# Kernel tuning notes

Measured on AMD Instinct MI355X. Metric: run time of the kernel, lower is better.

## Reference

```python
import jax, jax.numpy as jnp
import numpy as np

N, E = 50000, 800000
H, C_HID = 4, 64  # heads, hidden_units
C_IN, C_OUT = 256, 64
NEG_SLOPE = 0.2
EPS = 1e-16


def gat_conv(x, src, dst, W, att_src, att_dst, bias):
    """PyG GATConv with concat=False (mean over heads) + bias.
    x: [N, F_in], W: [F_in, H*C], att_*: [H, C], bias: [C]."""
    n = x.shape[0]
    h = (x @ W).reshape(n, H, -1)                     # [N, H, C]
    a_src = jnp.sum(h * att_src, axis=-1)             # [N, H]
    a_dst = jnp.sum(h * att_dst, axis=-1)             # [N, H]
    e = jax.nn.leaky_relu(a_src[src] + a_dst[dst], NEG_SLOPE)  # [E, H]
    # segment softmax grouped by destination node
    m = jax.ops.segment_max(e, dst, num_segments=n)   # [N, H]
    e = jnp.exp(e - m[dst])
    denom = jax.ops.segment_sum(e, dst, num_segments=n)
    alpha = e / (denom[dst] + EPS)                    # [E, H]
    msg = h[src] * alpha[:, :, None]                  # [E, H, C]
    out = jax.ops.segment_sum(msg, dst, num_segments=n)  # [N, H, C]
    return out.mean(axis=1) + bias                    # concat=False -> head mean


def setup_inputs() -> dict:
    key = jax.random.key(0)
    ks = jax.random.split(key, 16)
    inp = {
        "x": jax.random.normal(ks[0], (N, C_IN), dtype=jnp.float32),
        "edge_index": jax.random.randint(ks[1], (2, E), 0, N, dtype=jnp.int64),
    }
    dims = [(C_IN, C_HID), (C_HID, C_HID), (C_HID, C_OUT)]
    for i, (fi, fo) in enumerate(dims, start=1):
        inp[f"W{i}"] = jax.random.normal(ks[2 + 4 * (i - 1)], (fi, H * fo), dtype=jnp.float32) * (1.0 / np.sqrt(fi))
        inp[f"as{i}"] = jax.random.normal(ks[3 + 4 * (i - 1)], (H, fo), dtype=jnp.float32) * 0.1
        inp[f"ad{i}"] = jax.random.normal(ks[4 + 4 * (i - 1)], (H, fo), dtype=jnp.float32) * 0.1
        inp[f"b{i}"] = jnp.zeros((fo,), dtype=jnp.float32)
    return inp


def reference(x, edge_index, W1, as1, ad1, b1, W2, as2, ad2, b2, W3, as3, ad3, b3):
    n = x.shape[0]
    loop = jnp.arange(n, dtype=edge_index.dtype)
    src = jnp.concatenate([edge_index[0], loop])  # add_self_loops=True (PyG default)
    dst = jnp.concatenate([edge_index[1], loop])
    layers = [(W1, as1, ad1, b1), (W2, as2, ad2, b2), (W3, as3, ad3, b3)]
    for (W, a_s, a_d, b) in layers:
        x = gat_conv(x, src, dst, W, a_s, a_d, b)
        x = jax.nn.relu(x)  # dropout is identity at inference
    return jax.nn.log_softmax(x, axis=-1)
```

## Files before the change

### kernel.cpp

```cpp
#include <hip/hip_runtime.h>
#include <hip/hip_bf16.h>
#include <math.h>
#include <stdint.h>

#define HEADS 4
#define CH 64
#define HC 256
#define NEG 0.2f
#define EPSV 1e-16f
#define NEGBIG -3.0e38f

typedef __attribute__((ext_vector_type(8))) short short8;
typedef __attribute__((ext_vector_type(4))) float f32x4;
typedef _Float16 f16_t;
typedef __fp16 fp16x2 __attribute__((ext_vector_type(2)));

__device__ __forceinline__ float lrelu(float x) { return x > 0.f ? x : NEG * x; }

__device__ __forceinline__ unsigned short f2bf(float f) {
  __hip_bfloat16 b = __float2bfloat16(f);
  return *reinterpret_cast<unsigned short*>(&b);
}
__device__ __forceinline__ unsigned short f16b(float f) {
  return __builtin_bit_cast(unsigned short, (f16_t)f);
}
__device__ __forceinline__ float dot2acc(unsigned int a, unsigned int h, float acc) {
#if __has_builtin(__builtin_amdgcn_fdot2)
  return __builtin_amdgcn_fdot2(__builtin_bit_cast(fp16x2, a),
                                __builtin_bit_cast(fp16x2, h), acc, false);
#else
  fp16x2 av = __builtin_bit_cast(fp16x2, a);
  fp16x2 hv = __builtin_bit_cast(fp16x2, h);
  return acc + (float)av[0] * (float)hv[0] + (float)av[1] * (float)hv[1];
#endif
}

__global__ __launch_bounds__(256) void wprep3_k(const float* __restrict__ W0,
                                                const float* __restrict__ W1,
                                                const float* __restrict__ W2,
                                                unsigned short* __restrict__ T0,
                                                unsigned short* __restrict__ T1,
                                                unsigned short* __restrict__ T2) {
  int i = blockIdx.x * 256 + threadIdx.x;
  if (i < 65536) {
    int k = i >> 8, n = i & 255;
    T0[n * 256 + k] = f2bf(W0[i]);
  } else if (i < 81920) {
    int j = i - 65536, k = j >> 8, n = j & 255;
    T1[n * 64 + k] = f2bf(W1[j]);
  } else if (i < 98304) {
    int j = i - 81920, k = j >> 8, n = j & 255;
    T2[n * 64 + k] = f2bf(W2[j]);
  }
}

#define AS_STR 268
#define CS_STR 258
template <int K, int AF32>
__global__ __launch_bounds__(256, 4) void mfma_gat_k(const float* __restrict__ Af,
                                                     const unsigned short* __restrict__ Ab,
                                                     const unsigned short* __restrict__ Wt,
                                                     const float* __restrict__ att_s,
                                                     const float* __restrict__ att_d,
                                                     unsigned short* __restrict__ ht16,
                                                     float* __restrict__ a_src,
                                                     float* __restrict__ a_dst,
                                                     int M) {
  __shared__ unsigned short Sh[32 * AS_STR];

  int tid = threadIdx.x;
  int bm = blockIdx.x * 32;
  int w = tid >> 6, l = tid & 63;
  int lr = l & 15, lk = l >> 4;
  int row_s = tid >> 3, seg = tid & 7;
  bool rowok = (bm + row_s < M);

  if (AF32) {
    #pragma unroll 4
    for (int kq = 0; kq < K; kq += 32) {
      float4 v = make_float4(0.f, 0.f, 0.f, 0.f);
      if (rowok)
        v = *reinterpret_cast<const float4*>(Af + (size_t)(bm + row_s) * K + kq + seg * 4);
      ushort4 u;
      u.x = f2bf(v.x); u.y = f2bf(v.y); u.z = f2bf(v.z); u.w = f2bf(v.w);
      *reinterpret_cast<ushort4*>(&Sh[row_s * AS_STR + kq + seg * 4]) = u;
    }
  } else {
    #pragma unroll 4
    for (int kq = 0; kq < K; kq += 32) {
      ushort4 u = make_ushort4(0, 0, 0, 0);
      if (rowok)
        u = *reinterpret_cast<const ushort4*>(Ab + (size_t)(bm + row_s) * K + kq + seg * 4);
      *reinterpret_cast<ushort4*>(&Sh[row_s * AS_STR + kq + seg * 4]) = u;
    }
  }
  __syncthreads();

  f32x4 acc[2][4];
  #pragma unroll
  for (int rt = 0; rt < 2; ++rt)
    #pragma unroll
    for (int ct = 0; ct < 4; ++ct) {
      f32x4 z = {0.f, 0.f, 0.f, 0.f};
      acc[rt][ct] = z;
    }

  const unsigned short* wp0 = Wt + (size_t)(w * 64 + lr) * K + lk * 8;

  #pragma unroll 2
  for (int k0 = 0; k0 < K; k0 += 32) {
    short8 bfr[4];
    #pragma unroll
    for (int ct = 0; ct < 4; ++ct)
      bfr[ct] = *reinterpret_cast<const short8*>(wp0 + (size_t)ct * 16 * K + k0);
    #pragma unroll
    for (int rt = 0; rt < 2; ++rt) {
      short8 af = *reinterpret_cast<const short8*>(&Sh[(rt * 16 + lr) * AS_STR + k0 + lk * 8]);
      #pragma unroll
      for (int ct = 0; ct < 4; ++ct)
        acc[rt][ct] = __builtin_amdgcn_mfma_f32_16x16x32_bf16(af, bfr[ct], acc[rt][ct], 0, 0, 0);
    }
  }
  __syncthreads();

  #pragma unroll
  for (int rt = 0; rt < 2; ++rt)
    #pragma unroll
    for (int ct = 0; ct < 4; ++ct)
      #pragma unroll
      for (int r = 0; r < 4; ++r) {
        int row = rt * 16 + lk * 4 + r;
        int c = ct * 16 + lr;
        Sh[row * CS_STR + c * 4 + w] = f16b(acc[rt][ct][r]);
      }
  __syncthreads();

  if (rowok) {
    ushort4* dst = reinterpret_cast<ushort4*>(ht16 + (size_t)(bm + row_s) * HC + seg * 32);
    const unsigned short* srcp = &Sh[row_s * CS_STR + seg * 32];
    #pragma unroll
    for (int q = 0; q < 4; ++q)
      dst[q] = *reinterpret_cast<const ushort4*>(srcp + q * 4);
  }

  {
    int nd = tid >> 3, q = tid & 7, h = q >> 1, half = q & 1;
    float ps = 0.f, pd = 0.f;
    const float* ats = att_s + h * 64 + half * 32;
    const float* atd = att_d + h * 64 + half * 32;
    const unsigned short* cp = &Sh[nd * CS_STR + (half * 32) * 4 + h];
    #pragma unroll
    for (int c = 0; c < 32; ++c) {
      float hv = (float)__builtin_bit_cast(f16_t, cp[c * 4]);
      ps += hv * ats[c];
      pd += hv * atd[c];
    }
    ps += __shfl_xor(ps, 1);
    pd += __shfl_xor(pd, 1);
    if (!(q & 1) && bm + nd < M) {
      a_src[(size_t)(bm + nd) * 4 + h] = ps;
      a_dst[(size_t)(bm + nd) * 4 + h] = pd;
    }
  }
}

__global__ __launch_bounds__(256) void hist_k(const int* __restrict__ dst, int* __restrict__ count, int E) {
  int e = blockIdx.x * blockDim.x + threadIdx.x;
  if (e < E) atomicAdd(&count[dst[e]], 1);
}

__global__ __launch_bounds__(512) void scan1_k(const int* __restrict__ count,
                                               int* __restrict__ rp,
                                               int* __restrict__ bsum, int n) {
  __shared__ int sh[512];
  int tx = threadIdx.x;
  int i = blockIdx.x * 512 + tx;
  int v = (i < n) ? count[i] : 0;
  sh[tx] = v;
  __syncthreads();
  #pragma unroll
  for (int off = 1; off < 512; off <<= 1) {
    int t = (tx >= off) ? sh[tx - off] : 0;
    __syncthreads();
    sh[tx] += t;
    __syncthreads();
  }
  if (i < n) rp[i] = sh[tx] - v;
  if (tx == 511) bsum[blockIdx.x] = sh[511];
}

__global__ __launch_bounds__(128) void scan2_k(int* __restrict__ bsum, int nb) {
  __shared__ int sh[128];
  int tx = threadIdx.x;
  int v = (tx < nb) ? bsum[tx] : 0;
  sh[tx] = v;
  __syncthreads();
  #pragma unroll
  for (int off = 1; off < 128; off <<= 1) {
    int t = (tx >= off) ? sh[tx - off] : 0;
    __syncthreads();
    sh[tx] += t;
    __syncthreads();
  }
  if (tx < nb) bsum[tx] = sh[tx] - v;
}

__global__ __launch_bounds__(512) void scan3_k(int* __restrict__ rp, const int* __restrict__ bsum,
                                               int n, int E) {
  int i = blockIdx.x * 512 + threadIdx.x;
  if (i < n) rp[i] += bsum[blockIdx.x];
  if (i == 0) rp[n] = E;
}

__global__ __launch_bounds__(256) void scatter_k(const int* __restrict__ src, const int* __restrict__ dst,
                                                 const int* __restrict__ rp, int* __restrict__ cursor,
                                                 int* __restrict__ csr_src, int E) {
  int e = blockIdx.x * blockDim.x + threadIdx.x;
  if (e >= E) return;
  int d = dst[e];
  int pos = rp[d] + atomicAdd(&cursor[d], 1);
  csr_src[pos] = src[e];
}

__global__ __launch_bounds__(256) void soft_agg_k(const int* __restrict__ rp,
                                                  const int* __restrict__ csr_src,
                                                  const float* __restrict__ a_src,
                                                  const float* __restrict__ a_dst,
                                                  const unsigned short* __restrict__ ht16,
                                                  const float* __restrict__ bias,
                                                  float* __restrict__ outf,
                                                  unsigned short* __restrict__ outb,
                                                  int N, int do_lsm) {
  __shared__ uint4 rec[4][34];
  int tid  = threadIdx.x;
  int w    = tid >> 6;
  int lane = tid & 63;
  int wid  = (blockIdx.x * blockDim.x + tid) >> 6;
  if (wid >= N) return;
  int rs = rp[wid], re = rp[wid + 1];
  int ep = lane & 15;
  int h  = lane >> 4;

  float adh = a_dst[(size_t)wid * 4 + h];
  float ash = a_src[(size_t)wid * 4 + h];
  float es  = lrelu(ash + adh);

  int s0 = 0, s1 = 0;
  float e0 = NEGBIG, e1 = NEGBIG;
  if (rs + ep < re) {
    s0 = csr_src[rs + ep];
    e0 = lrelu(a_src[(size_t)s0 * 4 + h] + adh);
  }
  if (rs + 16 + ep < re) {
    s1 = csr_src[rs + 16 + ep];
    e1 = lrelu(a_src[(size_t)s1 * 4 + h] + adh);
  }
  float m = fmaxf(es, fmaxf(e0, e1));
  for (int base = rs + 32; base < re; base += 16) {
    if (base + ep < re) {
      int s = csr_src[base + ep];
      m = fmaxf(m, lrelu(a_src[(size_t)s * 4 + h] + adh));
    }
  }
  #pragma unroll
  for (int off = 8; off > 0; off >>= 1) m = fmaxf(m, __shfl_xor(m, off));

  float p0 = expf(e0 - m), p1 = expf(e1 - m);
  float dn = p0 + p1;
  for (int base = rs + 32; base < re; base += 16) {
    if (base + ep < re) {
      int s = csr_src[base + ep];
      dn += expf(lrelu(a_src[(size_t)s * 4 + h] + adh) - m);
    }
  }
  #pragma unroll
  for (int off = 8; off > 0; off >>= 1) dn += __shfl_xor(dn, off);
  float sp = expf(es - m);
  dn += sp;
  float rr = 1.f / (dn + EPSV);

  unsigned short* recb = reinterpret_cast<unsigned short*>(&rec[w][0]);
  float acc = 0.f;
  const unsigned short* hl = ht16 + lane * 4;

  auto agg = [&](int cnt) {
    int k = 0;
    for (; k + 4 <= cnt; k += 4) {
      uint4 r0 = rec[w][k + 0], r1 = rec[w][k + 1];
      uint4 r2 = rec[w][k + 2], r3 = rec[w][k + 3];
      int t0 = __builtin_amdgcn_readfirstlane((int)r0.z);
      int t1 = __builtin_amdgcn_readfirstlane((int)r1.z);
      int t2 = __builtin_amdgcn_readfirstlane((int)r2.z);
      int t3 = __builtin_amdgcn_readfirstlane((int)r3.z);
      uint2 h0 = *reinterpret_cast<const uint2*>(hl + (size_t)t0 * HC);
      uint2 h1 = *reinterpret_cast<const uint2*>(hl + (size_t)t1 * HC);
      uint2 h2 = *reinterpret_cast<const uint2*>(hl + (size_t)t2 * HC);
      uint2 h3 = *reinterpret_cast<const uint2*>(hl + (size_t)t3 * HC);
      acc = dot2acc(r0.x, h0.x, acc); acc = dot2acc(r0.y, h0.y, acc);
      acc = dot2acc(r1.x, h1.x, acc); acc = dot2acc(r1.y, h1.y, acc);
      acc = dot2acc(r2.x, h2.x, acc); acc = dot2acc(r2.y, h2.y, acc);
      acc = dot2acc(r3.x, h3.x, acc); acc = dot2acc(r3.y, h3.y, acc);
    }
    for (; k < cnt; ++k) {
      uint4 r0 = rec[w][k];
      int t0 = __builtin_amdgcn_readfirstlane((int)r0.z);
      uint2 hv = *reinterpret_cast<const uint2*>(hl + (size_t)t0 * HC);
      acc = dot2acc(r0.x, hv.x, acc);
      acc = dot2acc(r0.y, hv.y, acc);
    }
  };

  if (ep == 0) recb[32 * 8 + h] = f16b(sp * rr);
  recb[ep * 8 + h] = f16b(p0 * rr);
  recb[(16 + ep) * 8 + h] = f16b(p1 * rr);
  if (h == 0) {
    *reinterpret_cast<int*>(recb + ep * 8 + 4) = s0;
    *reinterpret_cast<int*>(recb + (16 + ep) * 8 + 4) = s1;
  }
  {
    int cnt = re - rs; if (cnt > 32) cnt = 32;
    agg(cnt);
  }
  for (int base = rs + 32; base < re; base += 16) {
    int s = 0;
    float e = NEGBIG;
    if (base + ep < re) {
      s = csr_src[base + ep];
      e = lrelu(a_src[(size_t)s * 4 + h] + adh);
    }
    recb[ep * 8 + h] = f16b(expf(e - m) * rr);
    if (h == 0) *reinterpret_cast<int*>(recb + ep * 8 + 4) = s;
    int cnt = re - base; if (cnt > 16) cnt = 16;
    agg(cnt);
  }

  uint2 sa = *reinterpret_cast<const uint2*>(&rec[w][32]);
  uint2 shv = *reinterpret_cast<const uint2*>(ht16 + (size_t)wid * HC + lane * 4);
  acc = dot2acc(sa.x, shv.x, acc);
  acc = dot2acc(sa.y, shv.y, acc);
  float v = acc * 0.25f + bias[lane];
  v = fmaxf(v, 0.f);
  if (do_lsm) {
    float mx = v;
    #pragma unroll
    for (int off = 32; off > 0; off >>= 1) mx = fmaxf(mx, __shfl_xor(mx, off));
    float ex = expf(v - mx);
    float sm = ex;
    #pragma unroll
    for (int off = 32; off > 0; off >>= 1) sm += __shfl_xor(sm, off);
    outf[(size_t)wid * CH + lane] = v - mx - logf(sm);
  } else {
    outb[(size_t)wid * CH + lane] = f2bf(v);
  }
}

extern "C" void kernel_launch(void* const* d_in, const int* in_sizes, int n_in,
                              void* d_out, int out_size, void* d_ws, size_t ws_size,
                              hipStream_t stream) {
  const float* x0 = (const float*)d_in[0];
  const int*   ei = (const int*)d_in[1];
  int N = in_sizes[0] / HC;
  int E = in_sizes[1] / 2;
  const int* srcp = ei;
  const int* dstp = ei + E;

  const float* W[3]  = {(const float*)d_in[2], (const float*)d_in[6],  (const float*)d_in[10]};
  const float* AS[3] = {(const float*)d_in[3], (const float*)d_in[7],  (const float*)d_in[11]};
  const float* AD[3] = {(const float*)d_in[4], (const float*)d_in[8],  (const float*)d_in[12]};
  const float* BI[3] = {(const float*)d_in[5], (const float*)d_in[9],  (const float*)d_in[13]};

  char* ws = (char*)d_ws;
  size_t off = 0;
  auto alloc = [&](size_t bytes) {
    void* p = ws + off;
    off += (bytes + 255) & ~(size_t)255;
    return p;
  };
  unsigned short* ht16    = (unsigned short*)alloc((size_t)N * HC * 2);
  unsigned short* xb16    = (unsigned short*)alloc((size_t)N * CH * 2);
  float*          a_s     = (float*)alloc((size_t)N * 4 * 4);
  float*          a_d     = (float*)alloc((size_t)N * 4 * 4);
  int*            rowp    = (int*)alloc((size_t)(N + 1) * 4);
  int*            cursor  = (int*)alloc((size_t)N * 4);
  int*            csr_src = (int*)alloc((size_t)E * 4);
  int*            bsum    = (int*)alloc(512 * 4);
  unsigned short* Wt[3];
  Wt[0] = (unsigned short*)alloc((size_t)256 * 256 * 2);
  Wt[1] = (unsigned short*)alloc((size_t)256 * 64 * 2);
  Wt[2] = (unsigned short*)alloc((size_t)256 * 64 * 2);

  wprep3_k<<<384, 256, 0, stream>>>(W[0], W[1], W[2], Wt[0], Wt[1], Wt[2]);

  int nb = (N + 511) / 512;
  hipMemsetAsync(rowp, 0, (size_t)((char*)(cursor + N) - (char*)rowp), stream);
  hist_k<<<(E + 255) / 256, 256, 0, stream>>>(dstp, rowp, E);
  scan1_k<<<nb, 512, 0, stream>>>(rowp, rowp, bsum, N);
  scan2_k<<<1, 128, 0, stream>>>(bsum, nb);
  scan3_k<<<nb, 512, 0, stream>>>(rowp, bsum, N, E);
  scatter_k<<<(E + 255) / 256, 256, 0, stream>>>(srcp, dstp, rowp, cursor, csr_src, E);

  int gblocks = (N + 31) / 32;
  for (int L = 0; L < 3; ++L) {
    if (L == 0)
      mfma_gat_k<256, 1><<<gblocks, 256, 0, stream>>>(x0, nullptr, Wt[0], AS[0], AD[0],
                                                      ht16, a_s, a_d, N);
    else
      mfma_gat_k<64, 0><<<gblocks, 256, 0, stream>>>(nullptr, xb16, Wt[L], AS[L], AD[L],
                                                     ht16, a_s, a_d, N);
    soft_agg_k<<<(N + 3) / 4, 256, 0, stream>>>(rowp, csr_src, a_s, a_d, ht16, BI[L],
                                                (float*)d_out, xb16, N, (L == 2) ? 1 : 0);
  }
}
```

Before: 383.8 us.

## Prefetch first 16 neighbor features before softmax reduction and fuse scan kernels

In the aggregation kernel, the feature rows of the first 16 neighbors are loaded into registers while the softmax denominator is still being computed. This overlaps the gather latency with the exp/reduction work. Those 16 neighbors are then accumulated with a static unrolled loop, and the remaining edges go through the dynamic LDS-record path. The CSR build also merges the block-sum scan and the offset-add kernels into one launch when the block count fits in 128, saving a launch. The costs are higher register pressure from 16 uint2 prefetches and unconditional loads for low-degree nodes (index 0 is used for padding).

```diff
diff --git a/kernel.cpp b/kernel.cpp
--- a/kernel.cpp
+++ b/kernel.cpp
@@ -189,6 +189,26 @@
   if (tx == 511) bsum[blockIdx.x] = sh[511];
 }
 
+__global__ __launch_bounds__(512) void scan23_k(int* __restrict__ rp, const int* __restrict__ bsum,
+                                                int nb, int n, int E) {
+  __shared__ int sh[128];
+  int tx = threadIdx.x;
+  if (tx < 128) sh[tx] = (tx < nb) ? bsum[tx] : 0;
+  __syncthreads();
+  #pragma unroll
+  for (int off = 1; off < 128; off <<= 1) {
+    int t = 0;
+    if (tx < 128 && tx >= off) t = sh[tx - off];
+    __syncthreads();
+    if (tx < 128) sh[tx] += t;
+    __syncthreads();
+  }
+  int add = (blockIdx.x == 0) ? 0 : sh[blockIdx.x - 1];
+  int i = blockIdx.x * 512 + tx;
+  if (i < n) rp[i] += add;
+  if (i == 0) rp[n] = E;
+}
+
 __global__ __launch_bounds__(128) void scan2_k(int* __restrict__ bsum, int nb) {
   __shared__ int sh[128];
   int tx = threadIdx.x;
@@ -231,7 +251,8 @@
                                                   float* __restrict__ outf,
                                                   unsigned short* __restrict__ outb,
                                                   int N, int do_lsm) {
-  __shared__ uint4 rec[4][34];
+  __shared__ __align__(16) unsigned short a0s[4][72];
+  __shared__ uint4 rec1[4][16];
   int tid  = threadIdx.x;
   int w    = tid >> 6;
   int lane = tid & 63;
@@ -265,6 +286,14 @@
   #pragma unroll
   for (int off = 8; off > 0; off >>= 1) m = fmaxf(m, __shfl_xor(m, off));
 
+  const unsigned short* hl = ht16 + lane * 4;
+  uint2 g[16];
+  #pragma unroll
+  for (int k = 0; k < 16; ++k) {
+    int t = __builtin_amdgcn_readlane(s0, k);
+    g[k] = *reinterpret_cast<const uint2*>(hl + (size_t)t * HC);
+  }
+
   float p0 = expf(e0 - m), p1 = expf(e1 - m);
   float dn = p0 + p1;
   for (int base = rs + 32; base < re; base += 16) {
@@ -279,15 +308,29 @@
   dn += sp;
   float rr = 1.f / (dn + EPSV);
 
-  unsigned short* recb = reinterpret_cast<unsigned short*>(&rec[w][0]);
+  a0s[w][ep * 4 + h] = f16b(p0 * rr);
+  if (ep == 0) a0s[w][64 + h] = f16b(sp * rr);
+
   float acc = 0.f;
-  const unsigned short* hl = ht16 + lane * 4;
-
-  auto agg = [&](int cnt) {
+  #pragma unroll
+  for (int k = 0; k < 16; ++k) {
+    uint2 q = *reinterpret_cast<const uint2*>(&a0s[w][k * 4]);
+    acc = dot2acc(q.x, g[k].x, acc);
+    acc = dot2acc(q.y, g[k].y, acc);
+  }
+  {
+    uint2 sa = *reinterpret_cast<const uint2*>(&a0s[w][64]);
+    uint2 shv = *reinterpret_cast<const uint2*>(ht16 + (size_t)wid * HC + lane * 4);
+    acc = dot2acc(sa.x, shv.x, acc);
+    acc = dot2acc(sa.y, shv.y, acc);
+  }
+
+  unsigned short* r1b = reinterpret_cast<unsigned short*>(&rec1[w][0]);
+  auto agg_dyn = [&](int cnt) {
     int k = 0;
     for (; k + 4 <= cnt; k += 4) {
-      uint4 r0 = rec[w][k + 0], r1 = rec[w][k + 1];
-      uint4 r2 = rec[w][k + 2], r3 = rec[w][k + 3];
+      uint4 r0 = rec1[w][k + 0], r1 = rec1[w][k + 1];
+      uint4 r2 = rec1[w][k + 2], r3 = rec1[w][k + 3];
       int t0 = __builtin_amdgcn_readfirstlane((int)r0.z);
       int t1 = __builtin_amdgcn_readfirstlane((int)r1.z);
       int t2 = __builtin_amdgcn_readfirstlane((int)r2.z);
@@ -302,7 +345,7 @@
       acc = dot2acc(r3.x, h3.x, acc); acc = dot2acc(r3.y, h3.y, acc);
     }
     for (; k < cnt; ++k) {
-      uint4 r0 = rec[w][k];
+      uint4 r0 = rec1[w][k];
       int t0 = __builtin_amdgcn_readfirstlane((int)r0.z);
       uint2 hv = *reinterpret_cast<const uint2*>(hl + (size_t)t0 * HC);
       acc = dot2acc(r0.x, hv.x, acc);
@@ -310,16 +353,11 @@
     }
   };
 
-  if (ep == 0) recb[32 * 8 + h] = f16b(sp * rr);
-  recb[ep * 8 + h] = f16b(p0 * rr);
-  recb[(16 + ep) * 8 + h] = f16b(p1 * rr);
-  if (h == 0) {
-    *reinterpret_cast<int*>(recb + ep * 8 + 4) = s0;
-    *reinterpret_cast<int*>(recb + (16 + ep) * 8 + 4) = s1;
-  }
-  {
-    int cnt = re - rs; if (cnt > 32) cnt = 32;
-    agg(cnt);
+  if (re > rs + 16) {
+    r1b[ep * 8 + h] = f16b(p1 * rr);
+    if (h == 0) *reinterpret_cast<int*>(r1b + ep * 8 + 4) = s1;
+    int cnt = re - rs - 16; if (cnt > 16) cnt = 16;
+    agg_dyn(cnt);
   }
   for (int base = rs + 32; base < re; base += 16) {
     int s = 0;
@@ -328,16 +366,12 @@
       s = csr_src[base + ep];
       e = lrelu(a_src[(size_t)s * 4 + h] + adh);
     }
-    recb[ep * 8 + h] = f16b(expf(e - m) * rr);
-    if (h == 0) *reinterpret_cast<int*>(recb + ep * 8 + 4) = s;
+    r1b[ep * 8 + h] = f16b(expf(e - m) * rr);
+    if (h == 0) *reinterpret_cast<int*>(r1b + ep * 8 + 4) = s;
     int cnt = re - base; if (cnt > 16) cnt = 16;
-    agg(cnt);
-  }
-
-  uint2 sa = *reinterpret_cast<const uint2*>(&rec[w][32]);
-  uint2 shv = *reinterpret_cast<const uint2*>(ht16 + (size_t)wid * HC + lane * 4);
-  acc = dot2acc(sa.x, shv.x, acc);
-  acc = dot2acc(sa.y, shv.y, acc);
+    agg_dyn(cnt);
+  }
+
   float v = acc * 0.25f + bias[lane];
   v = fmaxf(v, 0.f);
   if (do_lsm) {
@@ -395,8 +429,12 @@
   hipMemsetAsync(rowp, 0, (size_t)((char*)(cursor + N) - (char*)rowp), stream);
   hist_k<<<(E + 255) / 256, 256, 0, stream>>>(dstp, rowp, E);
   scan1_k<<<nb, 512, 0, stream>>>(rowp, rowp, bsum, N);
-  scan2_k<<<1, 128, 0, stream>>>(bsum, nb);
-  scan3_k<<<nb, 512, 0, stream>>>(rowp, bsum, N, E);
+  if (nb <= 128) {
+    scan23_k<<<nb, 512, 0, stream>>>(rowp, bsum, nb, N, E);
+  } else {
+    scan2_k<<<1, 128, 0, stream>>>(bsum, nb);
+    scan3_k<<<nb, 512, 0, stream>>>(rowp, bsum, N, E);
+  }
   scatter_k<<<(E + 255) / 256, 256, 0, stream>>>(srcp, dstp, rowp, cursor, csr_src, E);
 
   int gblocks = (N + 31) / 32;
```

Measured after the change: 394.1 us. 2.7% more time.

## Fuse neighbor aggregation with next-layer GEMM and merge scan kernels

Applied to the files above, without the earlier changes.

Each block now aggregates 32 destination nodes (8 per wave) into shared memory, then runs the next layer's bf16 MFMA projection and attention-logit computation in the same kernel. This removes the intermediate bf16 activation write/read and two launches per layer, using ping-pong buffers for features and logits. The scan's second and third passes are also merged into one kernel when the block count is small. In exchange, each wave processes nodes serially, which reduces the parallelism available to hide gather latency.

```diff
diff --git a/kernel.cpp b/kernel.cpp
--- a/kernel.cpp
+++ b/kernel.cpp
@@ -54,6 +54,117 @@
   }
 }
 
+__device__ __forceinline__ float soft_agg_node(int node, int N,
+                                               const int* __restrict__ rp,
+                                               const int* __restrict__ csr_src,
+                                               const float* __restrict__ a_src,
+                                               const float* __restrict__ a_dst,
+                                               const unsigned short* __restrict__ ht16,
+                                               uint4* recw,
+                                               int lane, int ep, int h) {
+  if (node >= N) return 0.f;
+  int rs = rp[node], re = rp[node + 1];
+
+  float adh = a_dst[(size_t)node * 4 + h];
+  float ash = a_src[(size_t)node * 4 + h];
+  float es  = lrelu(ash + adh);
+
+  int s0 = 0, s1 = 0;
+  float e0 = NEGBIG, e1 = NEGBIG;
+  if (rs + ep < re) {
+    s0 = csr_src[rs + ep];
+    e0 = lrelu(a_src[(size_t)s0 * 4 + h] + adh);
+  }
+  if (rs + 16 + ep < re) {
+    s1 = csr_src[rs + 16 + ep];
+    e1 = lrelu(a_src[(size_t)s1 * 4 + h] + adh);
+  }
+  float m = fmaxf(es, fmaxf(e0, e1));
+  for (int base = rs + 32; base < re; base += 16) {
+    if (base + ep < re) {
+      int s = csr_src[base + ep];
+      m = fmaxf(m, lrelu(a_src[(size_t)s * 4 + h] + adh));
+    }
+  }
+  #pragma unroll
+  for (int off = 8; off > 0; off >>= 1) m = fmaxf(m, __shfl_xor(m, off));
+
+  float p0 = expf(e0 - m), p1 = expf(e1 - m);
+  float dn = p0 + p1;
+  for (int base = rs + 32; base < re; base += 16) {
+    if (base + ep < re) {
+      int s = csr_src[base + ep];
+      dn += expf(lrelu(a_src[(size_t)s * 4 + h] + adh) - m);
+    }
+  }
+  #pragma unroll
+  for (int off = 8; off > 0; off >>= 1) dn += __shfl_xor(dn, off);
+  float sp = expf(es - m);
+  dn += sp;
+  float rr = 1.f / (dn + EPSV);
+
+  unsigned short* recb = reinterpret_cast<unsigned short*>(recw);
+  float acc = 0.f;
+  const unsigned short* hl = ht16 + lane * 4;
+
+  auto agg = [&](int cnt) {
+    int k = 0;
+    for (; k + 4 <= cnt; k += 4) {
+      uint4 r0 = recw[k + 0], r1 = recw[k + 1];
+      uint4 r2 = recw[k + 2], r3 = recw[k + 3];
+      int t0 = __builtin_amdgcn_readfirstlane((int)r0.z);
+      int t1 = __builtin_amdgcn_readfirstlane((int)r1.z);
+      int t2 = __builtin_amdgcn_readfirstlane((int)r2.z);
+      int t3 = __builtin_amdgcn_readfirstlane((int)r3.z);
+      uint2 h0 = *reinterpret_cast<const uint2*>(hl + (size_t)t0 * HC);
+      uint2 h1 = *reinterpret_cast<const uint2*>(hl + (size_t)t1 * HC);
+      uint2 h2 = *reinterpret_cast<const uint2*>(hl + (size_t)t2 * HC);
+      uint2 h3 = *reinterpret_cast<const uint2*>(hl + (size_t)t3 * HC);
+      acc = dot2acc(r0.x, h0.x, acc); acc = dot2acc(r0.y, h0.y, acc);
+      acc = dot2acc(r1.x, h1.x, acc); acc = dot2acc(r1.y, h1.y, acc);
+      acc = dot2acc(r2.x, h2.x, acc); acc = dot2acc(r2.y, h2.y, acc);
+      acc = dot2acc(r3.x, h3.x, acc); acc = dot2acc(r3.y, h3.y, acc);
+    }
+    for (; k < cnt; ++k) {
+      uint4 r0 = recw[k];
+      int t0 = __builtin_amdgcn_readfirstlane((int)r0.z);
+      uint2 hv = *reinterpret_cast<const uint2*>(hl + (size_t)t0 * HC);
+      acc = dot2acc(r0.x, hv.x, acc);
+      acc = dot2acc(r0.y, hv.y, acc);
+    }
+  };
+
+  if (ep == 0) recb[32 * 8 + h] = f16b(sp * rr);
+  recb[ep * 8 + h] = f16b(p0 * rr);
+  recb[(16 + ep) * 8 + h] = f16b(p1 * rr);
+  if (h == 0) {
+    *reinterpret_cast<int*>(recb + ep * 8 + 4) = s0;
+    *reinterpret_cast<int*>(recb + (16 + ep) * 8 + 4) = s1;
+  }
+  {
+    int cnt = re - rs; if (cnt > 32) cnt = 32;
+    agg(cnt);
+  }
+  for (int base = rs + 32; base < re; base += 16) {
+    int s = 0;
+    float e = NEGBIG;
+    if (base + ep < re) {
+      s = csr_src[base + ep];
+      e = lrelu(a_src[(size_t)s * 4 + h] + adh);
+    }
+    recb[ep * 8 + h] = f16b(expf(e - m) * rr);
+    if (h == 0) *reinterpret_cast<int*>(recb + ep * 8 + 4) = s;
+    int cnt = re - base; if (cnt > 16) cnt = 16;
+    agg(cnt);
+  }
+
+  uint2 sa = *reinterpret_cast<const uint2*>(&recw[32]);
+  uint2 shv = *reinterpret_cast<const uint2*>(ht16 + (size_t)node * HC + lane * 4);
+  acc = dot2acc(sa.x, shv.x, acc);
+  acc = dot2acc(sa.y, shv.y, acc);
+  return acc;
+}
+
 #define AS_STR 268
 #define CS_STR 258
 template <int K, int AF32>
@@ -164,6 +275,137 @@
   }
 }
 
+__global__ __launch_bounds__(256) void fused_agg_gemm_k(const int* __restrict__ rp,
+                                                        const int* __restrict__ csr_src,
+                                                        const float* __restrict__ as_in,
+                                                        const float* __restrict__ ad_in,
+                                                        const unsigned short* __restrict__ ht_in,
+                                                        const float* __restrict__ bias_in,
+                                                        const unsigned short* __restrict__ Wt_nx,
+                                                        const float* __restrict__ as_nx,
+                                                        const float* __restrict__ ad_nx,
+                                                        unsigned short* __restrict__ ht_out,
+                                                        float* __restrict__ as_out,
+                                                        float* __restrict__ ad_out,
+                                                        int N) {
+  __shared__ unsigned short Sh[32 * AS_STR];
+  __shared__ uint4 rec[4][34];
+
+  int tid = threadIdx.x;
+  int w = tid >> 6, lane = tid & 63;
+  int ep = lane & 15, h = lane >> 4;
+  int bm = blockIdx.x * 32;
+
+  #pragma unroll 1
+  for (int i = 0; i < 8; ++i) {
+    int node = bm + w * 8 + i;
+    float acc = soft_agg_node(node, N, rp, csr_src, as_in, ad_in, ht_in, &rec[w][0], lane, ep, h);
+    float v = fmaxf(acc * 0.25f + bias_in[lane], 0.f);
+    Sh[(w * 8 + i) * AS_STR + lane] = f2bf(v);
+  }
+  __syncthreads();
+
+  constexpr int K = 64;
+  int lr = lane & 15, lk = lane >> 4;
+  int row_s = tid >> 3, seg = tid & 7;
+  bool rowok = (bm + row_s < N);
+
+  f32x4 acc2[2][4];
+  #pragma unroll
+  for (int rt = 0; rt < 2; ++rt)
+    #pragma unroll
+    for (int ct = 0; ct < 4; ++ct) {
+      f32x4 z = {0.f, 0.f, 0.f, 0.f};
+      acc2[rt][ct] = z;
+    }
+
+  const unsigned short* wp0 = Wt_nx + (size_t)(w * 64 + lr) * K + lk * 8;
+
+  #pragma unroll
+  for (int k0 = 0; k0 < K; k0 += 32) {
+    short8 bfr[4];
+    #pragma unroll
+    for (int ct = 0; ct < 4; ++ct)
+      bfr[ct] = *reinterpret_cast<const short8*>(wp0 + (size_t)ct * 16 * K + k0);
+    #pragma unroll
+    for (int rt = 0; rt < 2; ++rt) {
+      short8 af = *reinterpret_cast<const short8*>(&Sh[(rt * 16 + lr) * AS_STR + k0 + lk * 8]);
+      #pragma unroll
+      for (int ct = 0; ct < 4; ++ct)
+        acc2[rt][ct] = __builtin_amdgcn_mfma_f32_16x16x32_bf16(af, bfr[ct], acc2[rt][ct], 0, 0, 0);
+    }
+  }
+  __syncthreads();
+
+  #pragma unroll
+  for (int rt = 0; rt < 2; ++rt)
+    #pragma unroll
+    for (int ct = 0; ct < 4; ++ct)
+      #pragma unroll
+      for (int r = 0; r < 4; ++r) {
+        int row = rt * 16 + lk * 4 + r;
+        int c = ct * 16 + lr;
+        Sh[row * CS_STR + c * 4 + w] = f16b(acc2[rt][ct][r]);
+      }
+  __syncthreads();
+
+  if (rowok) {
+    ushort4* dst = reinterpret_cast<ushort4*>(ht_out + (size_t)(bm + row_s) * HC + seg * 32);
+    const unsigned short* srcp = &Sh[row_s * CS_STR + seg * 32];
+    #pragma unroll
+    for (int q = 0; q < 4; ++q)
+      dst[q] = *reinterpret_cast<const ushort4*>(srcp + q * 4);
+  }
+
+  {
+    int nd = tid >> 3, q = tid & 7, hh = q >> 1, half = q & 1;
+    float ps = 0.f, pd = 0.f;
+    const float* ats = as_nx + hh * 64 + half * 32;
+    const float* atd = ad_nx + hh * 64 + half * 32;
+    const unsigned short* cp = &Sh[nd * CS_STR + (half * 32) * 4 + hh];
+    #pragma unroll
+    for (int c = 0; c < 32; ++c) {
+      float hv = (float)__builtin_bit_cast(f16_t, cp[c * 4]);
+      ps += hv * ats[c];
+      pd += hv * atd[c];
+    }
+    ps += __shfl_xor(ps, 1);
+    pd += __shfl_xor(pd, 1);
+    if (!(q & 1) && bm + nd < N) {
+      as_out[(size_t)(bm + nd) * 4 + hh] = ps;
+      ad_out[(size_t)(bm + nd) * 4 + hh] = pd;
+    }
+  }
+}
+
+__global__ __launch_bounds__(256) void soft_agg_lsm_k(const int* __restrict__ rp,
+                                                      const int* __restrict__ csr_src,
+                                                      const float* __restrict__ a_src,
+                                                      const float* __restrict__ a_dst,
+                                                      const unsigned short* __restrict__ ht16,
+                                                      const float* __restrict__ bias,
+                                                      float* __restrict__ outf,
+                                                      int N) {
+  __shared__ uint4 rec[4][34];
+  int tid = threadIdx.x;
+  int w = tid >> 6, lane = tid & 63;
+  int ep = lane & 15, h = lane >> 4;
+  int wid = (blockIdx.x * blockDim.x + tid) >> 6;
+  if (wid >= N) return;
+
+  float acc = soft_agg_node(wid, N, rp, csr_src, a_src, a_dst, ht16, &rec[w][0], lane, ep, h);
+  float v = fmaxf(acc * 0.25f + bias[lane], 0.f);
+
+  float mx = v;
+  #pragma unroll
+  for (int off = 32; off > 0; off >>= 1) mx = fmaxf(mx, __shfl_xor(mx, off));
+  float ex = expf(v - mx);
+  float sm = ex;
+  #pragma unroll
+  for (int off = 32; off > 0; off >>= 1) sm += __shfl_xor(sm, off);
+  outf[(size_t)wid * CH + lane] = v - mx - logf(sm);
+}
+
 __global__ __launch_bounds__(256) void hist_k(const int* __restrict__ dst, int* __restrict__ count, int E) {
   int e = blockIdx.x * blockDim.x + threadIdx.x;
   if (e < E) atomicAdd(&count[dst[e]], 1);
@@ -189,6 +431,26 @@
   if (tx == 511) bsum[blockIdx.x] = sh[511];
 }
 
+__global__ __launch_bounds__(512) void scan23_k(int* __restrict__ rp, const int* __restrict__ bsum,
+                                                int nb, int n, int E) {
+  __shared__ int sh[128];
+  int tx = threadIdx.x;
+  if (tx < 128) sh[tx] = (tx < nb) ? bsum[tx] : 0;
+  __syncthreads();
+  #pragma unroll
+  for (int off = 1; off < 128; off <<= 1) {
+    int t = 0;
+    if (tx < 128 && tx >= off) t = sh[tx - off];
+    __syncthreads();
+    if (tx < 128) sh[tx] += t;
+    __syncthreads();
+  }
+  int add = (blockIdx.x == 0) ? 0 : sh[blockIdx.x - 1];
+  int i = blockIdx.x * 512 + tx;
+  if (i < n) rp[i] += add;
+  if (i == 0) rp[n] = E;
+}
+
 __global__ __launch_bounds__(128) void scan2_k(int* __restrict__ bsum, int nb) {
   __shared__ int sh[128];
   int tx = threadIdx.x;
@@ -220,138 +482,6 @@
   int d = dst[e];
   int pos = rp[d] + atomicAdd(&cursor[d], 1);
   csr_src[pos] = src[e];
-}
-
-__global__ __launch_bounds__(256) void soft_agg_k(const int* __restrict__ rp,
-                                                  const int* __restrict__ csr_src,
-                                                  const float* __restrict__ a_src,
-                                                  const float* __restrict__ a_dst,
-                                                  const unsigned short* __restrict__ ht16,
-                                                  const float* __restrict__ bias,
-                                                  float* __restrict__ outf,
-                                                  unsigned short* __restrict__ outb,
-                                                  int N, int do_lsm) {
-  __shared__ uint4 rec[4][34];
-  int tid  = threadIdx.x;
-  int w    = tid >> 6;
-  int lane = tid & 63;
-  int wid  = (blockIdx.x * blockDim.x + tid) >> 6;
-  if (wid >= N) return;
-  int rs = rp[wid], re = rp[wid + 1];
-  int ep = lane & 15;
-  int h  = lane >> 4;
-
-  float adh = a_dst[(size_t)wid * 4 + h];
-  float ash = a_src[(size_t)wid * 4 + h];
-  float es  = lrelu(ash + adh);
-
-  int s0 = 0, s1 = 0;
-  float e0 = NEGBIG, e1 = NEGBIG;
-  if (rs + ep < re) {
-    s0 = csr_src[rs + ep];
-    e0 = lrelu(a_src[(size_t)s0 * 4 + h] + adh);
-  }
-  if (rs + 16 + ep < re) {
-    s1 = csr_src[rs + 16 + ep];
-    e1 = lrelu(a_src[(size_t)s1 * 4 + h] + adh);
-  }
-  float m = fmaxf(es, fmaxf(e0, e1));
-  for (int base = rs + 32; base < re; base += 16) {
-    if (base + ep < re) {
-      int s = csr_src[base + ep];
-      m = fmaxf(m, lrelu(a_src[(size_t)s * 4 + h] + adh));
-    }
-  }
-  #pragma unroll
-  for (int off = 8; off > 0; off >>= 1) m = fmaxf(m, __shfl_xor(m, off));
-
-  float p0 = expf(e0 - m), p1 = expf(e1 - m);
-  float dn = p0 + p1;
-  for (int base = rs + 32; base < re; base += 16) {
-    if (base + ep < re) {
-      int s = csr_src[base + ep];
-      dn += expf(lrelu(a_src[(size_t)s * 4 + h] + adh) - m);
-    }
-  }
-  #pragma unroll
-  for (int off = 8; off > 0; off >>= 1) dn += __shfl_xor(dn, off);
-  float sp = expf(es - m);
-  dn += sp;
-  float rr = 1.f / (dn + EPSV);
-
-  unsigned short* recb = reinterpret_cast<unsigned short*>(&rec[w][0]);
-  float acc = 0.f;
-  const unsigned short* hl = ht16 + lane * 4;
-
-  auto agg = [&](int cnt) {
-    int k = 0;
-    for (; k + 4 <= cnt; k += 4) {
-      uint4 r0 = rec[w][k + 0], r1 = rec[w][k + 1];
-      uint4 r2 = rec[w][k + 2], r3 = rec[w][k + 3];
-      int t0 = __builtin_amdgcn_readfirstlane((int)r0.z);
-      int t1 = __builtin_amdgcn_readfirstlane((int)r1.z);
-      int t2 = __builtin_amdgcn_readfirstlane((int)r2.z);
-      int t3 = __builtin_amdgcn_readfirstlane((int)r3.z);
-      uint2 h0 = *reinterpret_cast<const uint2*>(hl + (size_t)t0 * HC);
-      uint2 h1 = *reinterpret_cast<const uint2*>(hl + (size_t)t1 * HC);
-      uint2 h2 = *reinterpret_cast<const uint2*>(hl + (size_t)t2 * HC);
-      uint2 h3 = *reinterpret_cast<const uint2*>(hl + (size_t)t3 * HC);
-      acc = dot2acc(r0.x, h0.x, acc); acc = dot2acc(r0.y, h0.y, acc);
-      acc = dot2acc(r1.x, h1.x, acc); acc = dot2acc(r1.y, h1.y, acc);
-      acc = dot2acc(r2.x, h2.x, acc); acc = dot2acc(r2.y, h2.y, acc);
-      acc = dot2acc(r3.x, h3.x, acc); acc = dot2acc(r3.y, h3.y, acc);
-    }
-    for (; k < cnt; ++k) {
-      uint4 r0 = rec[w][k];
-      int t0 = __builtin_amdgcn_readfirstlane((int)r0.z);
-      uint2 hv = *reinterpret_cast<const uint2*>(hl + (size_t)t0 * HC);
-      acc = dot2acc(r0.x, hv.x, acc);
-      acc = dot2acc(r0.y, hv.y, acc);
-    }
-  };
-
-  if (ep == 0) recb[32 * 8 + h] = f16b(sp * rr);
-  recb[ep * 8 + h] = f16b(p0 * rr);
-  recb[(16 + ep) * 8 + h] = f16b(p1 * rr);
-  if (h == 0) {
-    *reinterpret_cast<int*>(recb + ep * 8 + 4) = s0;
-    *reinterpret_cast<int*>(recb + (16 + ep) * 8 + 4) = s1;
-  }
-  {
-    int cnt = re - rs; if (cnt > 32) cnt = 32;
-    agg(cnt);
-  }
-  for (int base = rs + 32; base < re; base += 16) {
-    int s = 0;
-    float e = NEGBIG;
-    if (base + ep < re) {
-      s = csr_src[base + ep];
-      e = lrelu(a_src[(size_t)s * 4 + h] + adh);
-    }
-    recb[ep * 8 + h] = f16b(expf(e - m) * rr);
-    if (h == 0) *reinterpret_cast<int*>(recb + ep * 8 + 4) = s;
-    int cnt = re - base; if (cnt > 16) cnt = 16;
-    agg(cnt);
-  }
-
-  uint2 sa = *reinterpret_cast<const uint2*>(&rec[w][32]);
-  uint2 shv = *reinterpret_cast<const uint2*>(ht16 + (size_t)wid * HC + lane * 4);
-  acc = dot2acc(sa.x, shv.x, acc);
-  acc = dot2acc(sa.y, shv.y, acc);
-  float v = acc * 0.25f + bias[lane];
-  v = fmaxf(v, 0.f);
-  if (do_lsm) {
-    float mx = v;
-    #pragma unroll
-    for (int off = 32; off > 0; off >>= 1) mx = fmaxf(mx, __shfl_xor(mx, off));
-    float ex = expf(v - mx);
-    float sm = ex;
-    #pragma unroll
-    for (int off = 32; off > 0; off >>= 1) sm += __shfl_xor(sm, off);
-    outf[(size_t)wid * CH + lane] = v - mx - logf(sm);
-  } else {
-    outb[(size_t)wid * CH + lane] = f2bf(v);
-  }
 }
 
 extern "C" void kernel_launch(void* const* d_in, const int* in_sizes, int n_in,
@@ -376,10 +506,12 @@
     off += (bytes + 255) & ~(size_t)255;
     return p;
   };
-  unsigned short* ht16    = (unsigned short*)alloc((size_t)N * HC * 2);
-  unsigned short* xb16    = (unsigned short*)alloc((size_t)N * CH * 2);
-  float*          a_s     = (float*)alloc((size_t)N * 4 * 4);
-  float*          a_d     = (float*)alloc((size_t)N * 4 * 4);
+  unsigned short* htA     = (unsigned short*)alloc((size_t)N * HC * 2);
+  unsigned short* htB     = (unsigned short*)alloc((size_t)N * HC * 2);
+  float*          asA     = (float*)alloc((size_t)N * 4 * 4);
+  float*          adA     = (float*)alloc((size_t)N * 4 * 4);
+  float*          asB     = (float*)alloc((size_t)N * 4 * 4);
+  float*          adB     = (float*)alloc((size_t)N * 4 * 4);
   int*            rowp    = (int*)alloc((size_t)(N + 1) * 4);
   int*            cursor  = (int*)alloc((size_t)N * 4);
   int*            csr_src = (int*)alloc((size_t)E * 4);
@@ -395,19 +527,21 @@
   hipMemsetAsync(rowp, 0, (size_t)((char*)(cursor + N) - (char*)rowp), stream);
   hist_k<<<(E + 255) / 256, 256, 0, stream>>>(dstp, rowp, E);
   scan1_k<<<nb, 512, 0, stream>>>(rowp, rowp, bsum, N);
-  scan2_k<<<1, 128, 0, stream>>>(bsum, nb);
-  scan3_k<<<nb, 512, 0, stream>>>(rowp, bsum, N, E);
+  if (nb <= 128) {
+    scan23_k<<<nb, 512, 0, stream>>>(rowp, bsum, nb, N, E);
+  } else {
+    scan2_k<<<1, 128, 0, stream>>>(bsum, nb);
+    scan3_k<<<nb, 512, 0, stream>>>(rowp, bsum, N, E);
+  }
   scatter_k<<<(E + 255) / 256, 256, 0, stream>>>(srcp, dstp, rowp, cursor, csr_src, E);
 
   int gblocks = (N + 31) / 32;
-  for (int L = 0; L < 3; ++L) {
-    if (L == 0)
-      mfma_gat_k<256, 1><<<gblocks, 256, 0, stream>>>(x0, nullptr, Wt[0], AS[0], AD[0],
-                                                      ht16, a_s, a_d, N);
-    else
-      mfma_gat_k<64, 0><<<gblocks, 256, 0, stream>>>(nullptr, xb16, Wt[L], AS[L], AD[L],
-                                                     ht16, a_s, a_d, N);
-    soft_agg_k<<<(N + 3) / 4, 256, 0, stream>>>(rowp, csr_src, a_s, a_d, ht16, BI[L],
-                                                (float*)d_out, xb16, N, (L == 2) ? 1 : 0);
-  }
-}
+  mfma_gat_k<256, 1><<<gblocks, 256, 0, stream>>>(x0, nullptr, Wt[0], AS[0], AD[0],
+                                                  htA, asA, adA, N);
+  fused_agg_gemm_k<<<gblocks, 256, 0, stream>>>(rowp, csr_src, asA, adA, htA, BI[0],
+                                                Wt[1], AS[1], AD[1], htB, asB, adB, N);
+  fused_agg_gemm_k<<<gblocks, 256, 0, stream>>>(rowp, csr_src, asB, adB, htB, BI[1],
+                                                Wt[2], AS[2], AD[2], htA, asA, adA, N);
+  soft_agg_lsm_k<<<(N + 3) / 4, 256, 0, stream>>>(rowp, csr_src, asA, adA, htA, BI[2],
+                                                  (float*)d_out, N);
+}
```

After: 408.9 us. 6.5% more time.
